# Optimization experiments

Measured on AMD Instinct MI355X. Metric: run time of the kernel, lower is better.

Reference implementation:

```python
import jax, jax.numpy as jnp
import numpy as np

N = 100000
F_IN = 128
HID = 256
NUM_CLASSES = 64
E = 1600000


def setup_inputs() -> dict:
    key = jax.random.key(0)
    ks = jax.random.split(key, 10)
    x = jax.random.normal(ks[0], (N, F_IN), dtype=jnp.float32)
    edge_index = jax.random.randint(ks[1], (2, E), 0, N, dtype=jnp.int32)
    edge_weight = jax.random.uniform(ks[2], (E,), dtype=jnp.float32)
    def glorot(k, shape):
        lim = np.sqrt(6.0 / (shape[0] + shape[1]))
        return jax.random.uniform(k, shape, jnp.float32, -lim, lim)
    W0 = glorot(ks[3], (F_IN, HID)); b0 = jnp.zeros((HID,), jnp.float32)
    W1 = glorot(ks[4], (HID, HID)); b1 = jnp.zeros((HID,), jnp.float32)
    W2 = glorot(ks[5], (HID, NUM_CLASSES)); b2 = jnp.zeros((NUM_CLASSES,), jnp.float32)
    return {"x": x, "edge_index": edge_index, "edge_weight": edge_weight,
            "W0": W0, "b0": b0, "W1": W1, "b1": b1, "W2": W2, "b2": b2}


def _gcn_norm(edge_index, edge_weight, n_nodes):
    # renormalization trick: add self-loops (weight 1), D^-1/2 A D^-1/2
    loop = jnp.arange(n_nodes, dtype=edge_index.dtype)
    src = jnp.concatenate([edge_index[0], loop])
    dst = jnp.concatenate([edge_index[1], loop])
    w = jnp.concatenate([edge_weight, jnp.ones((n_nodes,), edge_weight.dtype)])
    deg = jax.ops.segment_sum(w, dst, num_segments=n_nodes)
    d_inv_sqrt = jnp.where(deg > 0, jax.lax.rsqrt(jnp.maximum(deg, 1e-12)), 0.0)
    norm = d_inv_sqrt[src] * w * d_inv_sqrt[dst]
    return src, dst, norm


def _gcn_layer(x, src, dst, norm, W, b, act):
    h = x @ W                                  # [N, d_out] project first (cheap dense)
    msg = h[src] * norm[:, None]               # [E+N, d_out] gather + scale
    out = jax.ops.segment_sum(msg, dst, num_segments=x.shape[0]) + b
    return act(out) if act is not None else out


def reference(x, edge_index, edge_weight, W0, b0, W1, b1, W2, b2):
    n_nodes = x.shape[0]
    src, dst, norm = _gcn_norm(edge_index, edge_weight, n_nodes)
    # dropout is identity at inference (training=None)
    h = _gcn_layer(x, src, dst, norm, W0, b0, jax.nn.relu)
    h = _gcn_layer(h, src, dst, norm, W1, b1, jax.nn.relu)
    h = _gcn_layer(h, src, dst, norm, W2, b2, None)
    return h
```

## Files before the change

kernel.cpp:

```cpp
#include <hip/hip_runtime.h>

#define N_NODES 100000
#define F_IN 128
#define HID 256
#define NCLS 64
#define N_EDGES 1600000

typedef _Float16 f16;
typedef f16 half8 __attribute__((ext_vector_type(8)));
typedef f16 half4 __attribute__((ext_vector_type(4)));
typedef float f32x4 __attribute__((ext_vector_type(4)));
typedef unsigned long long u64;

#define FIXED_SCALE 67108864.0f

__global__ void k_init(unsigned long long* __restrict__ degp, int n) {
    int i = blockIdx.x * 256 + threadIdx.x;
    if (i < n) degp[i] = (unsigned long long)(1u << 26);
}

#define EB   6250
#define XB   12500
#define W0B  128
#define W1B  256
#define W2B  64
__global__ __launch_bounds__(256) void mega1(
        const int* __restrict__ dst, const float* __restrict__ ew,
        unsigned long long* __restrict__ degp, int* __restrict__ seq,
        const float* __restrict__ x, f16* __restrict__ xh,
        const float* __restrict__ W0, f16* __restrict__ Wt0,
        const float* __restrict__ W1, f16* __restrict__ Wt1,
        const float* __restrict__ W2, f16* __restrict__ Wt2) {
    int bid = blockIdx.x;
    int t = threadIdx.x;
    if (bid < EB) {
        int i = bid * 256 + t;
        if (i < N_EDGES) {
            unsigned long long c = (1ULL << 40) |
                (unsigned long long)__float2uint_rn(ew[i] * FIXED_SCALE);
            unsigned long long old = atomicAdd(&degp[dst[i]], c);
            seq[i] = (int)(old >> 40);
        }
    } else if (bid < EB + XB) {
        int i = (bid - EB) * 256 + t;
        if (i < N_NODES * (F_IN / 4)) {
            float4 v = *(const float4*)&x[(size_t)i * 4];
            half4 o;
            o[0] = (f16)v.x; o[1] = (f16)v.y; o[2] = (f16)v.z; o[3] = (f16)v.w;
            *(half4*)&xh[(size_t)i * 4] = o;
        }
    } else if (bid < EB + XB + W0B) {
        int i = (bid - EB - XB) * 256 + t;
        int k = i / HID, d = i % HID;
        Wt0[d * F_IN + k] = (f16)W0[i];
    } else if (bid < EB + XB + W0B + W1B) {
        int i = (bid - EB - XB - W0B) * 256 + t;
        int k = i / HID, d = i % HID;
        Wt1[d * HID + k] = (f16)W1[i];
    } else {
        int i = (bid - EB - XB - W0B - W1B) * 256 + t;
        int k = i / NCLS, d = i % NCLS;
        Wt2[d * HID + k] = (f16)W2[i];
    }
}

__global__ void k_scan1(const unsigned long long* __restrict__ degp,
                        int* __restrict__ cnt, float* __restrict__ dis,
                        float* __restrict__ selfnorm,
                        int* __restrict__ incl, int* __restrict__ bsum, int n) {
    __shared__ int s[256];
    int t = threadIdx.x;
    int i = blockIdx.x * 256 + t;
    int v = 0;
    if (i < n) {
        unsigned long long p = degp[i];
        v = (int)(p >> 40);
        cnt[i] = v;
        float deg = (float)(p & ((1ULL << 40) - 1)) * (1.0f / FIXED_SCALE);
        float d = rsqrtf(deg);
        dis[i] = d;
        selfnorm[i] = d * d;
    }
    s[t] = v;
    __syncthreads();
    #pragma unroll
    for (int off = 1; off < 256; off <<= 1) {
        int x = (t >= off) ? s[t - off] : 0;
        __syncthreads();
        s[t] += x;
        __syncthreads();
    }
    if (i < n) incl[i] = s[t];
    if (t == 255) bsum[blockIdx.x] = s[255];
}

__global__ void k_scan2(const int* __restrict__ bsum, int* __restrict__ boff, int nb) {
    __shared__ int s[512];
    int t = threadIdx.x;
    int v = (t < nb) ? bsum[t] : 0;
    s[t] = v;
    __syncthreads();
    #pragma unroll
    for (int off = 1; off < 512; off <<= 1) {
        int x = (t >= off) ? s[t - off] : 0;
        __syncthreads();
        s[t] += x;
        __syncthreads();
    }
    if (t < nb) boff[t] = s[t] - v;
}

__global__ void k_scan3(int* __restrict__ row, const int* __restrict__ cnt,
                        const int* __restrict__ boff, int n) {
    int i = blockIdx.x * 256 + threadIdx.x;
    if (i < n) row[i] = row[i] - cnt[i] + boff[i >> 8];
}

__global__ void k_place(const int* __restrict__ src, const int* __restrict__ dst,
                        const float* __restrict__ w, const int* __restrict__ seq,
                        const int* __restrict__ row, const float* __restrict__ dis,
                        int2* __restrict__ csr, int e) {
    int i = blockIdx.x * 256 + threadIdx.x;
    if (i < e) {
        int s = src[i], d = dst[i];
        float nw = dis[s] * w[i] * dis[d];
        int pos = row[d] + seq[i];
        csr[pos] = make_int2(s, __float_as_int(nw));
    }
}

template <int K, int DOUT, bool BIAS_RELU>
__global__ __launch_bounds__(256) void gemm_mfma(const f16* __restrict__ in,
                                                 const f16* __restrict__ Wt,
                                                 const float* __restrict__ bias,
                                                 f16* __restrict__ out,
                                                 int nNodes) {
    constexpr int BM = 128, BN = 64, BK = 32;
    constexpr int NB = DOUT / BN;
    constexpr int AP = 40;
    constexpr int CP = 72;
    constexpr int SMEM = (BM * AP + BN * AP) > (BM * CP) ? (BM * AP + BN * AP) : (BM * CP);
    __shared__ f16 smem[SMEM];
    f16* As = smem;
    f16* Bs = smem + BM * AP;

    const int nwg = gridDim.x;
    const int b = blockIdx.x;
    const int q = nwg >> 3, r = nwg & 7, xcd = b & 7;
    const int wk = (xcd < r ? xcd * (q + 1) : r * (q + 1) + (xcd - r) * q) + (b >> 3);
    const int bx = wk / NB, by = wk % NB;

    const int t = threadIdx.x;
    const int w = t >> 6;
    const int lane = t & 63;
    const int quad = lane >> 4;
    const int l16 = lane & 15;
    const int nodeBase = bx * BM;
    const int colBase = by * BN;

    f32x4 acc[2][4] = {};

    for (int k0 = 0; k0 < K; k0 += BK) {
        {
            int koff = (t & 3) * 8;
            #pragma unroll
            for (int p = 0; p < 2; ++p) {
                int r2 = (t >> 2) + p * 64;
                int gn = nodeBase + r2;
                if (gn >= nNodes) gn = nNodes - 1;
                half8 v = *(const half8*)&in[(size_t)gn * K + k0 + koff];
                *(half8*)&As[r2 * AP + koff] = v;
            }
        }
        {
            int koff = (t & 3) * 8;
            int c = t >> 2;
            half8 v = *(const half8*)&Wt[(size_t)(colBase + c) * K + k0 + koff];
            *(half8*)&Bs[c * AP + koff] = v;
        }
        __syncthreads();

        half8 a[2];
        #pragma unroll
        for (int rt = 0; rt < 2; ++rt)
            a[rt] = *(const half8*)&As[(w * 32 + rt * 16 + l16) * AP + quad * 8];
        #pragma unroll
        for (int ct = 0; ct < 4; ++ct) {
            half8 bf = *(const half8*)&Bs[(ct * 16 + l16) * AP + quad * 8];
            acc[0][ct] = __builtin_amdgcn_mfma_f32_16x16x32_f16(a[0], bf, acc[0][ct], 0, 0, 0);
            acc[1][ct] = __builtin_amdgcn_mfma_f32_16x16x32_f16(a[1], bf, acc[1][ct], 0, 0, 0);
        }
        __syncthreads();
    }

    float bv[4];
    #pragma unroll
    for (int ct = 0; ct < 4; ++ct)
        bv[ct] = BIAS_RELU ? bias[colBase + ct * 16 + l16] : 0.0f;

    f16* Cs = smem;
    #pragma unroll
    for (int rt = 0; rt < 2; ++rt)
        #pragma unroll
        for (int ct = 0; ct < 4; ++ct)
            #pragma unroll
            for (int rr2 = 0; rr2 < 4; ++rr2) {
                int rr = w * 32 + rt * 16 + quad * 4 + rr2;
                int cc = ct * 16 + l16;
                float v = acc[rt][ct][rr2];
                if (BIAS_RELU) v = fmaxf(v + bv[ct], 0.0f);
                Cs[rr * CP + cc] = (f16)v;
            }
    __syncthreads();
    #pragma unroll
    for (int p = 0; p < 4; ++p) {
        int rr = (t >> 3) + p * 32;
        int gn = nodeBase + rr;
        int chunk = (t & 7) * 8;
        if (gn < nNodes)
            *(half8*)&out[(size_t)gn * DOUT + colBase + chunk] =
                *(const half8*)&Cs[rr * CP + chunk];
    }
}

template <int DOUT, int TPN, bool HAS_BIAS, bool OUT_F32>
__global__ __launch_bounds__(256) void agg_csr(const f16* __restrict__ h,
                                               const int2* __restrict__ csr,
                                               const int* __restrict__ row,
                                               const int* __restrict__ cnt,
                                               const float* __restrict__ sn,
                                               const float* __restrict__ bias,
                                               void* __restrict__ outv, int nNodes) {
    constexpr int NPB = 256 / TPN;
    int node = blockIdx.x * NPB + threadIdx.x / TPN;
    if (node >= nNodes) return;
    int lane = threadIdx.x % TPN;
    int col = lane * 8;

    float s = sn[node];
    half8 hv = *(const half8*)&h[(size_t)node * DOUT + col];
    float acc[8];
    #pragma unroll
    for (int i = 0; i < 8; ++i)
        acc[i] = s * (float)hv[i] + (HAS_BIAS ? bias[col + i] : 0.0f);

    int e = row[node];
    int end = e + cnt[node];

    for (; e + 3 < end; e += 4) {
        int2 e0 = csr[e], e1 = csr[e + 1], e2 = csr[e + 2], e3 = csr[e + 3];
        float w0 = __int_as_float(e0.y), w1 = __int_as_float(e1.y);
        float w2 = __int_as_float(e2.y), w3 = __int_as_float(e3.y);
        half8 a0 = *(const half8*)&h[(size_t)e0.x * DOUT + col];
        half8 a1 = *(const half8*)&h[(size_t)e1.x * DOUT + col];
        half8 a2 = *(const half8*)&h[(size_t)e2.x * DOUT + col];
        half8 a3 = *(const half8*)&h[(size_t)e3.x * DOUT + col];
        #pragma unroll
        for (int i = 0; i < 8; ++i)
            acc[i] += w0 * (float)a0[i] + w1 * (float)a1[i]
                    + w2 * (float)a2[i] + w3 * (float)a3[i];
    }
    for (; e + 1 < end; e += 2) {
        int2 e0 = csr[e], e1 = csr[e + 1];
        float w0 = __int_as_float(e0.y), w1 = __int_as_float(e1.y);
        half8 a0 = *(const half8*)&h[(size_t)e0.x * DOUT + col];
        half8 a1 = *(const half8*)&h[(size_t)e1.x * DOUT + col];
        #pragma unroll
        for (int i = 0; i < 8; ++i) acc[i] += w0 * (float)a0[i] + w1 * (float)a1[i];
    }
    if (e < end) {
        int2 e0 = csr[e];
        float w0 = __int_as_float(e0.y);
        half8 a0 = *(const half8*)&h[(size_t)e0.x * DOUT + col];
        #pragma unroll
        for (int i = 0; i < 8; ++i) acc[i] += w0 * (float)a0[i];
    }

    if (OUT_F32) {
        float* out = (float*)outv;
        float4 r0 = make_float4(acc[0], acc[1], acc[2], acc[3]);
        float4 r1 = make_float4(acc[4], acc[5], acc[6], acc[7]);
        *(float4*)&out[(size_t)node * DOUT + col] = r0;
        *(float4*)&out[(size_t)node * DOUT + col + 4] = r1;
    } else {
        f16* out = (f16*)outv;
        half8 o;
        #pragma unroll
        for (int i = 0; i < 8; ++i) o[i] = (f16)acc[i];
        *(half8*)&out[(size_t)node * DOUT + col] = o;
    }
}

extern "C" void kernel_launch(void* const* d_in, const int* in_sizes, int n_in,
                              void* d_out, int out_size, void* d_ws, size_t ws_size,
                              hipStream_t stream) {
    const float* x  = (const float*)d_in[0];
    const int*   ei = (const int*)d_in[1];
    const float* ew = (const float*)d_in[2];
    const float* W0 = (const float*)d_in[3];
    const float* b0 = (const float*)d_in[4];
    const float* W1 = (const float*)d_in[5];
    const float* b1 = (const float*)d_in[6];
    const float* W2 = (const float*)d_in[7];
    const float* b2 = (const float*)d_in[8];
    const int* src = ei;
    const int* dst = ei + N_EDGES;
    float* outp = (float*)d_out;

    char* ws = (char*)d_ws;
    unsigned long long* degp = (unsigned long long*)ws;  ws += N_NODES * 8;
    int2*  csr      = (int2*)ws;   ws += (size_t)N_EDGES * 8;
    int*   seq      = (int*)ws;    ws += (size_t)N_EDGES * 4;
    float* dis      = (float*)ws;  ws += N_NODES * 4;
    float* selfnorm = (float*)ws;  ws += N_NODES * 4;
    int*   cnt      = (int*)ws;    ws += N_NODES * 4;
    int*   row      = (int*)ws;    ws += N_NODES * 4;
    int*   bsum     = (int*)ws;    ws += 512 * 4;
    int*   boff     = (int*)ws;    ws += 512 * 4;
    f16*   xh       = (f16*)ws;    ws += (size_t)N_NODES * F_IN * 2;
    f16*   Wt0      = (f16*)ws;    ws += F_IN * HID * 2;
    f16*   Wt1      = (f16*)ws;    ws += HID * HID * 2;
    f16*   Wt2      = (f16*)ws;    ws += HID * NCLS * 2;
    f16*   bufA     = (f16*)ws;    ws += (size_t)N_NODES * HID * 2;
    f16*   bufB     = (f16*)ws;    ws += (size_t)N_NODES * HID * 2;

    const int nb = (N_NODES + 255) / 256;
    const int eb = (N_EDGES + 255) / 256;

    k_init<<<nb, 256, 0, stream>>>(degp, N_NODES);
    mega1<<<EB + XB + W0B + W1B + W2B, 256, 0, stream>>>(
        dst, ew, degp, seq, x, xh, W0, Wt0, W1, Wt1, W2, Wt2);
    k_scan1<<<nb, 256, 0, stream>>>(degp, cnt, dis, selfnorm, row, bsum, N_NODES);
    k_scan2<<<1, 512, 0, stream>>>(bsum, boff, nb);
    k_scan3<<<nb, 256, 0, stream>>>(row, cnt, boff, N_NODES);
    k_place<<<eb, 256, 0, stream>>>(src, dst, ew, seq, row, dis, csr, N_EDGES);

    const int gX = (N_NODES + 127) / 128;

    agg_csr<F_IN, 16, false, false><<<(N_NODES + 15) / 16, 256, 0, stream>>>(
        xh, csr, row, cnt, selfnorm, nullptr, bufA, N_NODES);
    gemm_mfma<F_IN, HID, true><<<gX * (HID / 64), 256, 0, stream>>>(bufA, Wt0, b0, bufB, N_NODES);

    agg_csr<HID, 32, false, false><<<(N_NODES + 7) / 8, 256, 0, stream>>>(
        bufB, csr, row, cnt, selfnorm, nullptr, bufA, N_NODES);
    gemm_mfma<HID, HID, true><<<gX * (HID / 64), 256, 0, stream>>>(bufA, Wt1, b1, bufB, N_NODES);

    gemm_mfma<HID, NCLS, false><<<gX * (NCLS / 64), 256, 0, stream>>>(bufB, Wt2, nullptr, bufA, N_NODES);
    agg_csr<NCLS, 8, true, true><<<(N_NODES + 31) / 32, 256, 0, stream>>>(
        bufA, csr, row, cnt, selfnorm, b2, outp, N_NODES);
}
```

Measured before the change: 519.3 us.

## Fuse CSR aggregation with MFMA GEMM for first two GCN layers

Adds a kernel that aggregates a 64-node tile of neighbor features into shared memory, then multiplies it by the weight matrix with MFMA and writes the biased ReLU output directly. This removes the intermediate aggregated buffer's global write and re-read, and two kernel launches, for layers 0 and 1. It also drops the 4-way edge unroll in the standalone aggregation. The trade-offs are a large LDS footprint that limits occupancy, B operand reads straight from global memory, and a serialized gather-then-compute phase within each block.

```diff
diff --git a/kernel.cpp b/kernel.cpp
--- a/kernel.cpp
+++ b/kernel.cpp
@@ -129,6 +129,100 @@
     }
 }
 
+template <int K, int DOUT, int TPN>
+__global__ __launch_bounds__(256, 3) void fused_agg_gemm(
+        const f16* __restrict__ h, const int2* __restrict__ csr,
+        const int* __restrict__ row, const int* __restrict__ cnt,
+        const float* __restrict__ sn, const f16* __restrict__ Wt,
+        const float* __restrict__ bias, f16* __restrict__ out, int nNodes) {
+    constexpr int BM = 64;
+    constexpr int MX = (K > DOUT) ? K : DOUT;
+    constexpr int AP = MX + 8;
+    __shared__ __attribute__((aligned(16))) f16 As[BM * AP];
+
+    const int t = threadIdx.x;
+    const int nodeBase = blockIdx.x * BM;
+
+    constexpr int NPB = 256 / TPN;
+    const int laneg = t % TPN;
+    const int sub = t / TPN;
+    const int col = laneg * 8;
+    #pragma unroll
+    for (int g = 0; g < BM / NPB; ++g) {
+        int rloc = g * NPB + sub;
+        int node = nodeBase + rloc;
+        if (node < nNodes) {
+            float s = sn[node];
+            half8 hv = *(const half8*)&h[(size_t)node * K + col];
+            float acc[8];
+            #pragma unroll
+            for (int i = 0; i < 8; ++i) acc[i] = s * (float)hv[i];
+
+            int e = row[node];
+            int end = e + cnt[node];
+            for (; e + 1 < end; e += 2) {
+                int2 e0 = csr[e], e1 = csr[e + 1];
+                float w0 = __int_as_float(e0.y), w1 = __int_as_float(e1.y);
+                half8 a0 = *(const half8*)&h[(size_t)e0.x * K + col];
+                half8 a1 = *(const half8*)&h[(size_t)e1.x * K + col];
+                #pragma unroll
+                for (int i = 0; i < 8; ++i)
+                    acc[i] += w0 * (float)a0[i] + w1 * (float)a1[i];
+            }
+            if (e < end) {
+                int2 e0 = csr[e];
+                float w0 = __int_as_float(e0.y);
+                half8 a0 = *(const half8*)&h[(size_t)e0.x * K + col];
+                #pragma unroll
+                for (int i = 0; i < 8; ++i) acc[i] += w0 * (float)a0[i];
+            }
+            half8 o;
+            #pragma unroll
+            for (int i = 0; i < 8; ++i) o[i] = (f16)acc[i];
+            *(half8*)&As[rloc * AP + col] = o;
+        }
+    }
+    __syncthreads();
+
+    const int w = t >> 6;
+    const int lane = t & 63;
+    const int quad = lane >> 4;
+    const int l16 = lane & 15;
+    constexpr int NCT = DOUT / 16;
+    f32x4 acc2[NCT] = {};
+
+    for (int k0 = 0; k0 < K; k0 += 32) {
+        half8 a = *(const half8*)&As[(w * 16 + l16) * AP + k0 + quad * 8];
+        #pragma unroll
+        for (int ct = 0; ct < NCT; ++ct) {
+            half8 b = *(const half8*)&Wt[(size_t)(ct * 16 + l16) * K + k0 + quad * 8];
+            acc2[ct] = __builtin_amdgcn_mfma_f32_16x16x32_f16(a, b, acc2[ct], 0, 0, 0);
+        }
+    }
+    __syncthreads();
+
+    #pragma unroll
+    for (int ct = 0; ct < NCT; ++ct) {
+        float bv = bias[ct * 16 + l16];
+        #pragma unroll
+        for (int r = 0; r < 4; ++r) {
+            int rr = w * 16 + quad * 4 + r;
+            As[rr * AP + ct * 16 + l16] = (f16)fmaxf(acc2[ct][r] + bv, 0.0f);
+        }
+    }
+    __syncthreads();
+    constexpr int CH = DOUT / 8;
+    #pragma unroll
+    for (int p = 0; p < BM * CH / 256; ++p) {
+        int idx = p * 256 + t;
+        int r = idx / CH, c8 = idx % CH;
+        int gn = nodeBase + r;
+        if (gn < nNodes)
+            *(half8*)&out[(size_t)gn * DOUT + c8 * 8] =
+                *(const half8*)&As[r * AP + c8 * 8];
+    }
+}
+
 template <int K, int DOUT, bool BIAS_RELU>
 __global__ __launch_bounds__(256) void gemm_mfma(const f16* __restrict__ in,
                                                  const f16* __restrict__ Wt,
@@ -247,19 +341,6 @@
     int e = row[node];
     int end = e + cnt[node];
 
-    for (; e + 3 < end; e += 4) {
-        int2 e0 = csr[e], e1 = csr[e + 1], e2 = csr[e + 2], e3 = csr[e + 3];
-        float w0 = __int_as_float(e0.y), w1 = __int_as_float(e1.y);
-        float w2 = __int_as_float(e2.y), w3 = __int_as_float(e3.y);
-        half8 a0 = *(const half8*)&h[(size_t)e0.x * DOUT + col];
-        half8 a1 = *(const half8*)&h[(size_t)e1.x * DOUT + col];
-        half8 a2 = *(const half8*)&h[(size_t)e2.x * DOUT + col];
-        half8 a3 = *(const half8*)&h[(size_t)e3.x * DOUT + col];
-        #pragma unroll
-        for (int i = 0; i < 8; ++i)
-            acc[i] += w0 * (float)a0[i] + w1 * (float)a1[i]
-                    + w2 * (float)a2[i] + w3 * (float)a3[i];
-    }
     for (; e + 1 < end; e += 2) {
         int2 e0 = csr[e], e1 = csr[e + 1];
         float w0 = __int_as_float(e0.y), w1 = __int_as_float(e1.y);
@@ -335,17 +416,16 @@
     k_scan3<<<nb, 256, 0, stream>>>(row, cnt, boff, N_NODES);
     k_place<<<eb, 256, 0, stream>>>(src, dst, ew, seq, row, dis, csr, N_EDGES);
 
+    const int gF = (N_NODES + 63) / 64;
     const int gX = (N_NODES + 127) / 128;
 
-    agg_csr<F_IN, 16, false, false><<<(N_NODES + 15) / 16, 256, 0, stream>>>(
-        xh, csr, row, cnt, selfnorm, nullptr, bufA, N_NODES);
-    gemm_mfma<F_IN, HID, true><<<gX * (HID / 64), 256, 0, stream>>>(bufA, Wt0, b0, bufB, N_NODES);
-
-    agg_csr<HID, 32, false, false><<<(N_NODES + 7) / 8, 256, 0, stream>>>(
-        bufB, csr, row, cnt, selfnorm, nullptr, bufA, N_NODES);
-    gemm_mfma<HID, HID, true><<<gX * (HID / 64), 256, 0, stream>>>(bufA, Wt1, b1, bufB, N_NODES);
-
-    gemm_mfma<HID, NCLS, false><<<gX * (NCLS / 64), 256, 0, stream>>>(bufB, Wt2, nullptr, bufA, N_NODES);
+    fused_agg_gemm<F_IN, HID, 16><<<gF, 256, 0, stream>>>(
+        xh, csr, row, cnt, selfnorm, Wt0, b0, bufB, N_NODES);
+
+    fused_agg_gemm<HID, HID, 32><<<gF, 256, 0, stream>>>(
+        bufB, csr, row, cnt, selfnorm, Wt1, b1, bufA, N_NODES);
+
+    gemm_mfma<HID, NCLS, false><<<gX * (NCLS / 64), 256, 0, stream>>>(bufA, Wt2, nullptr, bufB, N_NODES);
     agg_csr<NCLS, 8, true, true><<<(N_NODES + 31) / 32, 256, 0, stream>>>(
-        bufA, csr, row, cnt, selfnorm, b2, outp, N_NODES);
-}
+        bufB, csr, row, cnt, selfnorm, b2, outp, N_NODES);
+}
```

New measurement: 741.3 us. +42.7%, slower.
